# Kernel optimization log

Hardware: AMD Instinct MI355X
Metric: run time of the kernel (lower is better)

## Reference

```python
import jax, jax.numpy as jnp
import numpy as np

G, S, D, H, E = 8, 2048, 1024, 4096, 8  # groups, group_size, d_model, ffn_hidden, experts


def setup_inputs() -> dict:
    key = jax.random.key(0)
    ks = jax.random.split(key, 6)
    s = 0.02
    return {
        "x": jax.random.normal(ks[0], (G, S, D), dtype=jnp.float32),
        "gate_w": jax.random.normal(ks[1], (D, E), dtype=jnp.float32) * s,
        "ew1": jax.random.normal(ks[2], (E, D, H), dtype=jnp.float32) * s,
        "eb1": jnp.zeros((E, H), dtype=jnp.float32),
        "ew2": jax.random.normal(ks[3], (E, H, D), dtype=jnp.float32) * s,
        "eb2": jnp.zeros((E, D), dtype=jnp.float32),
        "sw1": jax.random.normal(ks[4], (D, H), dtype=jnp.float32) * s,
        "sb1": jnp.zeros((H,), dtype=jnp.float32),
        "sw2": jax.random.normal(ks[5], (H, D), dtype=jnp.float32) * s,
        "sb2": jnp.zeros((D,), dtype=jnp.float32),
        "expert_capacity": 2048,
    }


def reference(x, gate_w, ew1, eb1, ew2, eb2, sw1, sb1, sw2, sb2, expert_capacity):
    g, s_, d = x.shape
    e = gate_w.shape[1]
    T = g * s_
    cap = int(expert_capacity)

    # ---- Router (inference path) ----
    router_logits = jnp.einsum('gsd,de->gse', x, gate_w)           # (G,S,E)
    router_probs = jax.nn.softmax(router_logits, axis=-1)
    flat_probs = router_probs.transpose(2, 0, 1).reshape(e, T)      # (E,T)
    pad_w = max(0, cap - T)
    if pad_w > 0:
        flat_probs = jnp.pad(flat_probs, ((0, 0), (0, pad_w)),
                             mode='constant', constant_values=-1e9)
    scores, token_indices = jax.lax.top_k(flat_probs, k=cap)        # (E,C)
    scores = jnp.where(scores > -1e8, scores, 0.0)

    # ---- Routed experts: gather -> grouped FFN -> scale -> scatter-add ----
    x_flat = x.reshape(T, d)                                        # (T,D)
    safe_idx = jnp.clip(token_indices, 0, T - 1)                    # guard padded slots
    toks = x_flat[safe_idx]                                         # (E,C,D)
    h = jax.nn.gelu(jnp.einsum('ecd,edh->ech', toks, ew1) + eb1[:, None, :])
    y = jnp.einsum('ech,ehd->ecd', h, ew2) + eb2[:, None, :]        # (E,C,D)
    y = y * scores[..., None]                                       # zero weight kills padded slots
    routed = jnp.zeros_like(x_flat).at[safe_idx.reshape(-1)].add(y.reshape(-1, d))

    # ---- Shared expert over all tokens ----
    shared = jax.nn.gelu(x_flat @ sw1 + sb1) @ sw2 + sb2            # (T,D)

    return (routed + shared).reshape(g, s_, d)
```

## Files before the change

### kernel.cpp

```cpp
#include <hip/hip_runtime.h>

typedef __bf16 bf16;
typedef __bf16 bf16x8 __attribute__((ext_vector_type(8)));
typedef float f32x4 __attribute__((ext_vector_type(4)));

#define NTOK 16384
#define DMODEL 1024
#define HFFN 4096
#define NEXP 8
#define CAP 2048

#define VMCNT(n) asm volatile("s_waitcnt vmcnt(" #n ")" ::: "memory")
#define LGKM0() do { asm volatile("s_waitcnt lgkmcnt(0)" ::: "memory"); \
                     __builtin_amdgcn_sched_barrier(0); } while (0)
#define BARRIER() __builtin_amdgcn_s_barrier()

__device__ __forceinline__ void gload16(const void* g, void* l) {
  __builtin_amdgcn_global_load_lds((const __attribute__((address_space(1))) void*)g,
                                   (__attribute__((address_space(3))) void*)l, 16, 0, 0);
}

__device__ __forceinline__ float gelu_f(float v) {
  float t = v * v;
  float s2 = v * fmaf(0.10294358f, t, 2.3022084f);
  float e = __builtin_exp2f(-s2);
  return v * __builtin_amdgcn_rcpf(1.0f + e);
}

__device__ __forceinline__ void xcd_remap(int& bx, int& by) {
  const int gx = gridDim.x;
  const int lg = 31 - __clz((unsigned)gx);
  const int w = blockIdx.x + gx * blockIdx.y;
  bx = (w >> 3) & (gx - 1);
  by = (w & 7) | (((w >> 3) >> lg) << 3);
}

__global__ __launch_bounds__(256) void cvt_x_kernel(const float* __restrict__ x,
                                                    bf16* __restrict__ xb) {
  int i = blockIdx.x * blockDim.x + threadIdx.x;
  const float4* a = (const float4*)x + (size_t)i * 2;
  float4 v0 = a[0], v1 = a[1];
  bf16x8 o;
  o[0]=(bf16)v0.x; o[1]=(bf16)v0.y; o[2]=(bf16)v0.z; o[3]=(bf16)v0.w;
  o[4]=(bf16)v1.x; o[5]=(bf16)v1.y; o[6]=(bf16)v1.z; o[7]=(bf16)v1.w;
  *(bf16x8*)(xb + (size_t)i * 8) = o;
}

__global__ __launch_bounds__(64) void router_kernel(const float* __restrict__ x,
                                                    const float* __restrict__ gw,
                                                    float* __restrict__ probs) {
  int t = blockIdx.x;
  int l = threadIdx.x;
  int e = l & 7, chunk = l >> 3;
  const float* xr = x + (size_t)t * DMODEL + chunk * 128;
  const float* gwr = gw + (size_t)(chunk * 128) * NEXP + e;
  float a0 = 0.f, a1 = 0.f;
  #pragma unroll
  for (int d = 0; d < 128; d += 8) {
    float4 xv = *(const float4*)(xr + d);
    float4 xw = *(const float4*)(xr + d + 4);
    a0 += xv.x * gwr[(d+0)*8] + xv.y * gwr[(d+1)*8] + xv.z * gwr[(d+2)*8] + xv.w * gwr[(d+3)*8];
    a1 += xw.x * gwr[(d+4)*8] + xw.y * gwr[(d+5)*8] + xw.z * gwr[(d+6)*8] + xw.w * gwr[(d+7)*8];
  }
  float acc = a0 + a1;
  acc += __shfl_xor(acc, 8);
  acc += __shfl_xor(acc, 16);
  acc += __shfl_xor(acc, 32);
  float m = acc;
  m = fmaxf(m, __shfl_xor(m, 1));
  m = fmaxf(m, __shfl_xor(m, 2));
  m = fmaxf(m, __shfl_xor(m, 4));
  float ex = expf(acc - m);
  float s = ex;
  s += __shfl_xor(s, 1); s += __shfl_xor(s, 2); s += __shfl_xor(s, 4);
  if (l < 8) probs[(size_t)e * NTOK + t] = ex / s;
}

__global__ __launch_bounds__(256) void topk_kernel(const float* __restrict__ probs,
                                                   int* __restrict__ oidx,
                                                   float* __restrict__ oscr) {
  const int e = blockIdx.x;
  const float* p = probs + (size_t)e * NTOK;
  const int t = threadIdx.x;
  __shared__ unsigned hist[256];
  __shared__ unsigned sg[256], sq[256];
  __shared__ unsigned bcast[4];
  unsigned pref = 0, krem = CAP;
  for (int pass = 0; pass < 4; ++pass) {
    const int sh = 24 - pass * 8;
    hist[t] = 0;
    __syncthreads();
    for (int j = 0; j < 64; ++j) {
      unsigned u = __float_as_uint(p[t * 64 + j]);
      bool ok = (pass == 0) || ((u >> (sh + 8)) == pref);
      if (ok) atomicAdd(&hist[(u >> sh) & 255u], 1u);
    }
    __syncthreads();
    if (t == 0) {
      unsigned cum = 0; int b = 255;
      for (; b > 0; --b) {
        unsigned c = hist[b];
        if (cum + c >= krem) break;
        cum += c;
      }
      bcast[0] = (pref << 8) | (unsigned)b;
      bcast[1] = krem - cum;
    }
    __syncthreads();
    pref = bcast[0];
    krem = bcast[1];
  }
  const unsigned thr = pref;
  const unsigned neq_take = krem;
  unsigned cgt = 0, ceq = 0;
  for (int j = 0; j < 64; ++j) {
    unsigned u = __float_as_uint(p[t * 64 + j]);
    cgt += (u > thr);
    ceq += (u == thr);
  }
  sg[t] = cgt; sq[t] = ceq;
  __syncthreads();
  if (t == 0) {
    unsigned ag = 0, aq = 0;
    for (int i = 0; i < 256; ++i) {
      unsigned g = sg[i], q = sq[i];
      sg[i] = ag; sq[i] = aq;
      ag += g; aq += q;
    }
    bcast[2] = ag;
  }
  __syncthreads();
  const unsigned ngt = bcast[2];
  unsigned og = sg[t], oq = sq[t];
  int* oi = oidx + e * CAP;
  float* os = oscr + e * CAP;
  for (int j = 0; j < 64; ++j) {
    int tok = t * 64 + j;
    float pv = p[tok];
    unsigned u = __float_as_uint(pv);
    if (u > thr) {
      oi[og] = tok; os[og] = pv; ++og;
    } else if (u == thr) {
      if (oq < neq_take) { oi[ngt + oq] = tok; os[ngt + oq] = pv; }
      ++oq;
    }
  }
}

__global__ __launch_bounds__(256) void transpose_cvt(const float* __restrict__ in_e,
                                                     const float* __restrict__ in_s,
                                                     bf16* __restrict__ outp,
                                                     int R, int C) {
  int z = blockIdx.z;
  const float* in = (z < 8) ? (in_e + (size_t)z * (size_t)R * C) : in_s;
  bf16* out = outp + (size_t)z * (size_t)R * C;
  __shared__ float tile[64][65];
  int tx = threadIdx.x & 63, ty = threadIdx.x >> 6;
  int c0 = blockIdx.x * 64, r0 = blockIdx.y * 64;
  #pragma unroll
  for (int j = 0; j < 16; ++j) {
    int r = ty + j * 4;
    tile[r][tx] = in[(size_t)(r0 + r) * C + c0 + tx];
  }
  __syncthreads();
  #pragma unroll
  for (int j = 0; j < 16; ++j) {
    int c = ty + j * 4;
    out[(size_t)(c0 + c) * R + r0 + tx] = (bf16)tile[tx][c];
  }
}


#define STAGE_TILE_ALL(tt) do { \
  bf16* D_ = smem + (((tt) & 1) << 15); \
  const int ko_ = (tt) * 64; \
  gload16(srcA0 + ko_, D_ + tid8); \
  gload16(srcA1 + ko_, D_ + 4096 + tid8); \
  gload16(srcA2 + ko_, D_ + 8192 + tid8); \
  gload16(srcA3 + ko_, D_ + 12288 + tid8); \
  gload16(srcB0 + ko_, D_ + 16384 + tid8); \
  gload16(srcB1 + ko_, D_ + 20480 + tid8); \
  gload16(srcB2 + ko_, D_ + 24576 + tid8); \
  gload16(srcB3 + ko_, D_ + 28672 + tid8); \
} while (0)

#define KLOOP8(NT) do { \
  STAGE_TILE_ALL(0); \
  {  \
    bf16* D_ = smem + 32768; \
    gload16(srcA0 + 64, D_ + tid8); \
    gload16(srcA2 + 64, D_ + 8192 + tid8); \
    gload16(srcB0 + 64, D_ + 16384 + tid8); \
    gload16(srcB1 + 64, D_ + 20480 + tid8); \
    gload16(srcB2 + 64, D_ + 24576 + tid8); \
    gload16(srcB3 + 64, D_ + 28672 + tid8); \
  } \
  VMCNT(6); \
  BARRIER(); \
  for (int t = 0; t < (NT); ++t) { \
    const bf16* Ab_ = smem + ((t & 1) << 15); \
    const bf16* Bb_ = Ab_ + 16384; \
    bf16* Scur = smem + ((t & 1) << 15); \
    bf16* Snxt = smem + (((t + 1) & 1) << 15); \
    const int ko1 = (t + 1) * 64, ko2 = (t + 2) * 64; \
    const bool st1 = (t + 1) < (NT), st2 = (t + 2) < (NT); \
    bf16x8 aA[8], aB[8]; \
     \
    _Pragma("unroll") for (int i = 0; i < 4; ++i) { \
      aA[i*2+0] = *(const bf16x8*)(Ab_ + (wr*128 + i*16 + fr)*64 + c0s); \
      aA[i*2+1] = *(const bf16x8*)(Ab_ + (wr*128 + i*16 + fr)*64 + c1s); \
    } \
    _Pragma("unroll") for (int j = 0; j < 2; ++j) { \
      aB[j*2+0] = *(const bf16x8*)(Bb_ + (wc*64 + j*16 + fr)*64 + c0s); \
      aB[j*2+1] = *(const bf16x8*)(Bb_ + (wc*64 + j*16 + fr)*64 + c1s); \
    } \
    if (st1) { \
      gload16(srcA1 + ko1, Snxt + 4096 + tid8); \
      gload16(srcA3 + ko1, Snxt + 12288 + tid8); \
    } \
    BARRIER(); LGKM0(); \
    __builtin_amdgcn_s_setprio(1); \
    _Pragma("unroll") for (int i = 0; i < 4; ++i) \
      _Pragma("unroll") for (int j = 0; j < 2; ++j) { \
        acc[i][j] = __builtin_amdgcn_mfma_f32_16x16x32_bf16(aA[i*2+0], aB[j*2+0], acc[i][j], 0, 0, 0); \
        acc[i][j] = __builtin_amdgcn_mfma_f32_16x16x32_bf16(aA[i*2+1], aB[j*2+1], acc[i][j], 0, 0, 0); \
      } \
    __builtin_amdgcn_s_setprio(0); \
     \
    _Pragma("unroll") for (int j = 0; j < 2; ++j) { \
      aB[4+j*2+0] = *(const bf16x8*)(Bb_ + (wc*64 + 32 + j*16 + fr)*64 + c0s); \
      aB[4+j*2+1] = *(const bf16x8*)(Bb_ + (wc*64 + 32 + j*16 + fr)*64 + c1s); \
    } \
    BARRIER(); LGKM0(); \
    __builtin_amdgcn_s_setprio(1); \
    _Pragma("unroll") for (int i = 0; i < 4; ++i) \
      _Pragma("unroll") for (int j = 0; j < 2; ++j) { \
        acc[i][2+j] = __builtin_amdgcn_mfma_f32_16x16x32_bf16(aA[i*2+0], aB[4+j*2+0], acc[i][2+j], 0, 0, 0); \
        acc[i][2+j] = __builtin_amdgcn_mfma_f32_16x16x32_bf16(aA[i*2+1], aB[4+j*2+1], acc[i][2+j], 0, 0, 0); \
      } \
    __builtin_amdgcn_s_setprio(0); \
     \
    _Pragma("unroll") for (int i = 0; i < 4; ++i) { \
      aA[i*2+0] = *(const bf16x8*)(Ab_ + (wr*128 + 64 + i*16 + fr)*64 + c0s); \
      aA[i*2+1] = *(const bf16x8*)(Ab_ + (wr*128 + 64 + i*16 + fr)*64 + c1s); \
    } \
    if (st2) { \
      gload16(srcA0 + ko2, Scur + tid8); \
      gload16(srcA2 + ko2, Scur + 8192 + tid8); \
    } \
    BARRIER(); LGKM0(); \
    __builtin_amdgcn_s_setprio(1); \
    _Pragma("unroll") for (int i = 0; i < 4; ++i) \
      _Pragma("unroll") for (int j = 0; j < 2; ++j) { \
        acc[4+i][j] = __builtin_amdgcn_mfma_f32_16x16x32_bf16(aA[i*2+0], aB[j*2+0], acc[4+i][j], 0, 0, 0); \
        acc[4+i][j] = __builtin_amdgcn_mfma_f32_16x16x32_bf16(aA[i*2+1], aB[j*2+1], acc[4+i][j], 0, 0, 0); \
      } \
    __builtin_amdgcn_s_setprio(0); \
     \
    if (st2) { \
      gload16(srcB0 + ko2, Scur + 16384 + tid8); \
      gload16(srcB1 + ko2, Scur + 20480 + tid8); \
      gload16(srcB2 + ko2, Scur + 24576 + tid8); \
      gload16(srcB3 + ko2, Scur + 28672 + tid8); \
    } \
    if (st2) { VMCNT(6); } else { VMCNT(0); } \
    BARRIER(); \
    __builtin_amdgcn_s_setprio(1); \
    _Pragma("unroll") for (int i = 0; i < 4; ++i) \
      _Pragma("unroll") for (int j = 0; j < 2; ++j) { \
        acc[4+i][2+j] = __builtin_amdgcn_mfma_f32_16x16x32_bf16(aA[i*2+0], aB[4+j*2+0], acc[4+i][2+j], 0, 0, 0); \
        acc[4+i][2+j] = __builtin_amdgcn_mfma_f32_16x16x32_bf16(aA[i*2+1], aB[4+j*2+1], acc[4+i][2+j], 0, 0, 0); \
      } \
    __builtin_amdgcn_s_setprio(0); \
  } \
} while (0)

__global__ __launch_bounds__(512, 2) void ffn1_gemm(const bf16* __restrict__ xb,
                                                    const bf16* __restrict__ w1t,
                                                    const float* __restrict__ bias1,
                                                    const int* __restrict__ sel,
                                                    bf16* __restrict__ hout,
                                                    int routed) {
  const int e = blockIdx.z;
  const bf16* Bw = w1t + (routed ? (size_t)e * HFFN * DMODEL : 0);
  const float* bias = bias1 + (routed ? (size_t)e * HFFN : 0);
  bf16* hb = hout + (routed ? (size_t)e * CAP * HFFN : 0);
  int bx, by;
  xcd_remap(bx, by);
  const int m0 = by * 256, n0 = bx * 256;
  __shared__ __align__(16) bf16 smem[65536];
  const int tid = threadIdx.x, lane = tid & 63, wave = tid >> 6;
  const int wr = wave >> 2, wc = wave & 3;
  const int tid8 = tid * 8;

  const int srow = tid >> 3, sch = tid & 7;
  const int schs = sch ^ (srow & 7);
  const bf16 *srcA0, *srcA1, *srcA2, *srcA3, *srcB0, *srcB1, *srcB2, *srcB3;
  {
    int ra0 = routed ? sel[e * CAP + m0 + srow]       : (m0 + srow);
    int ra1 = routed ? sel[e * CAP + m0 + 64 + srow]  : (m0 + 64 + srow);
    int ra2 = routed ? sel[e * CAP + m0 + 128 + srow] : (m0 + 128 + srow);
    int ra3 = routed ? sel[e * CAP + m0 + 192 + srow] : (m0 + 192 + srow);
    srcA0 = xb + (size_t)ra0 * DMODEL + schs * 8;
    srcA1 = xb + (size_t)ra1 * DMODEL + schs * 8;
    srcA2 = xb + (size_t)ra2 * DMODEL + schs * 8;
    srcA3 = xb + (size_t)ra3 * DMODEL + schs * 8;
    srcB0 = Bw + (size_t)(n0 + srow) * DMODEL + schs * 8;
    srcB1 = Bw + (size_t)(n0 + 64 + srow) * DMODEL + schs * 8;
    srcB2 = Bw + (size_t)(n0 + 128 + srow) * DMODEL + schs * 8;
    srcB3 = Bw + (size_t)(n0 + 192 + srow) * DMODEL + schs * 8;
  }

  f32x4 acc[8][4];
  #pragma unroll
  for (int i = 0; i < 8; ++i)
    #pragma unroll
    for (int j = 0; j < 4; ++j) acc[i][j] = (f32x4){0.f, 0.f, 0.f, 0.f};

  const int fr = lane & 15;
  const int k8 = lane >> 4;
  const int sw = lane & 7;
  const int c0s = (k8 ^ sw) * 8;
  const int c1s = ((k8 + 4) ^ sw) * 8;

  KLOOP8(DMODEL / 64);

  __syncthreads();
  #pragma unroll
  for (int half = 0; half < 2; ++half) {
    if (wr == half) {
      #pragma unroll
      for (int i = 0; i < 8; ++i) {
        #pragma unroll
        for (int j = 0; j < 4; ++j) {
          const int nl = wc * 64 + j * 16 + fr;
          const float bb = bias[n0 + nl];
          #pragma unroll
          for (int q = 0; q < 4; ++q) {
            const int ml = i * 16 + (lane >> 4) * 4 + q;
            smem[ml * 256 + (nl ^ (((ml >> 2) & 7) << 4))] =
                (bf16)gelu_f(acc[i][j][q] + bb);
          }
        }
      }
    }
    __syncthreads();
    #pragma unroll
    for (int p = 0; p < 8; ++p) {
      const int flat = p * 512 + tid;
      const int row = flat >> 5, nc8 = flat & 31;
      uint4 v = *(const uint4*)(smem + row * 256 + ((nc8 * 8) ^ (((row >> 2) & 7) << 4)));
      *(uint4*)(hb + (size_t)(m0 + half * 128 + row) * HFFN + n0 + nc8 * 8) = v;
    }
    __syncthreads();
  }
}

__global__ __launch_bounds__(512, 2) void ffn2_gemm(const bf16* __restrict__ hbuf,
                                                    const bf16* __restrict__ w2t,
                                                    const float* __restrict__ bias2,
                                                    const int* __restrict__ sel,
                                                    const float* __restrict__ scr,
                                                    float* __restrict__ out,
                                                    int routed) {
  const int e = blockIdx.z;
  const bf16* Ab = hbuf + (routed ? (size_t)e * CAP * HFFN : 0);
  const bf16* Bw = w2t + (routed ? (size_t)e * DMODEL * HFFN : 0);
  const float* bias = bias2 + (routed ? (size_t)e * DMODEL : 0);
  int bx, by;
  xcd_remap(bx, by);
  const int m0 = by * 256, n0 = bx * 256;
  __shared__ __align__(16) bf16 smem[65536];
  __shared__ int s_tok[256];
  __shared__ float s_scl[256];
  const int tid = threadIdx.x, lane = tid & 63, wave = tid >> 6;
  const int wr = wave >> 2, wc = wave & 3;
  const int tid8 = tid * 8;

  const int srow = tid >> 3, sch = tid & 7;
  const int schs = sch ^ (srow & 7);
  const bf16* srcA0 = Ab + (size_t)(m0 + srow) * HFFN + schs * 8;
  const bf16* srcA1 = Ab + (size_t)(m0 + 64 + srow) * HFFN + schs * 8;
  const bf16* srcA2 = Ab + (size_t)(m0 + 128 + srow) * HFFN + schs * 8;
  const bf16* srcA3 = Ab + (size_t)(m0 + 192 + srow) * HFFN + schs * 8;
  const bf16* srcB0 = Bw + (size_t)(n0 + srow) * HFFN + schs * 8;
  const bf16* srcB1 = Bw + (size_t)(n0 + 64 + srow) * HFFN + schs * 8;
  const bf16* srcB2 = Bw + (size_t)(n0 + 128 + srow) * HFFN + schs * 8;
  const bf16* srcB3 = Bw + (size_t)(n0 + 192 + srow) * HFFN + schs * 8;
  if (routed && tid < 256) {
    s_tok[tid] = sel[e * CAP + m0 + tid];
    s_scl[tid] = scr[e * CAP + m0 + tid];
  }

  f32x4 acc[8][4];
  #pragma unroll
  for (int i = 0; i < 8; ++i)
    #pragma unroll
    for (int j = 0; j < 4; ++j) acc[i][j] = (f32x4){0.f, 0.f, 0.f, 0.f};

  const int fr = lane & 15;
  const int k8 = lane >> 4;
  const int sw = lane & 7;
  const int c0s = (k8 ^ sw) * 8;
  const int c1s = ((k8 + 4) ^ sw) * 8;

  KLOOP8(HFFN / 64);

  if (!routed) {
    #pragma unroll
    for (int i = 0; i < 8; ++i) {
      #pragma unroll
      for (int j = 0; j < 4; ++j) {
        const int nl = wc * 64 + j * 16 + fr;
        const float bb = bias[n0 + nl];
        #pragma unroll
        for (int q = 0; q < 4; ++q) {
          const int ml = wr * 128 + i * 16 + (lane >> 4) * 4 + q;
          out[(size_t)(m0 + ml) * DMODEL + n0 + nl] = acc[i][j][q] + bb;
        }
      }
    }
  } else {
    __syncthreads();
    #pragma unroll
    for (int i = 0; i < 8; ++i) {
      #pragma unroll
      for (int j = 0; j < 4; ++j) {
        const int nl = wc * 64 + j * 16 + fr;
        const float bb = bias[n0 + nl];
        #pragma unroll
        for (int q = 0; q < 4; ++q) {
          const int ml = wr * 128 + i * 16 + (lane >> 4) * 4 + q;
          const int tok = s_tok[ml];
          const float sc = s_scl[ml];
          atomicAdd(out + (size_t)tok * DMODEL + n0 + nl, (acc[i][j][q] + bb) * sc);
        }
      }
    }
  }
}

extern "C" void kernel_launch(void* const* d_in, const int* in_sizes, int n_in,
                              void* d_out, int out_size, void* d_ws, size_t ws_size,
                              hipStream_t stream) {
  const float* x   = (const float*)d_in[0];
  const float* gw  = (const float*)d_in[1];
  const float* ew1 = (const float*)d_in[2];
  const float* eb1 = (const float*)d_in[3];
  const float* ew2 = (const float*)d_in[4];
  const float* eb2 = (const float*)d_in[5];
  const float* sw1 = (const float*)d_in[6];
  const float* sb1 = (const float*)d_in[7];
  const float* sw2 = (const float*)d_in[8];
  const float* sb2 = (const float*)d_in[9];
  float* out = (float*)d_out;

  char* ws = (char*)d_ws;
  size_t off = 0;
  bf16* xb      = (bf16*)(ws + off); off += (size_t)NTOK * DMODEL * 2;
  bf16* w1t     = (bf16*)(ws + off); off += (size_t)9 * HFFN * DMODEL * 2;
  bf16* w2t     = (bf16*)(ws + off); off += (size_t)9 * DMODEL * HFFN * 2;
  bf16* hbuf    = (bf16*)(ws + off); off += (size_t)NTOK * HFFN * 2;
  float* probs  = (float*)(ws + off); off += (size_t)NEXP * NTOK * 4;
  int* selidx   = (int*)(ws + off);   off += (size_t)NEXP * CAP * 4;
  float* selscr = (float*)(ws + off); off += (size_t)NEXP * CAP * 4;

  cvt_x_kernel<<<dim3(NTOK * DMODEL / 8 / 256), dim3(256), 0, stream>>>(x, xb);
  router_kernel<<<dim3(NTOK), dim3(64), 0, stream>>>(x, gw, probs);
  topk_kernel<<<dim3(NEXP), dim3(256), 0, stream>>>(probs, selidx, selscr);
  transpose_cvt<<<dim3(HFFN / 64, DMODEL / 64, 9), dim3(256), 0, stream>>>(ew1, sw1, w1t, DMODEL, HFFN);
  transpose_cvt<<<dim3(DMODEL / 64, HFFN / 64, 9), dim3(256), 0, stream>>>(ew2, sw2, w2t, HFFN, DMODEL);

  ffn1_gemm<<<dim3(HFFN / 256, NTOK / 256, 1), dim3(512), 0, stream>>>(
      xb, w1t + (size_t)8 * HFFN * DMODEL, sb1, (const int*)nullptr, hbuf, 0);
  ffn2_gemm<<<dim3(DMODEL / 256, NTOK / 256, 1), dim3(512), 0, stream>>>(
      hbuf, w2t + (size_t)8 * DMODEL * HFFN, sb2, (const int*)nullptr, (const float*)nullptr, out, 0);

  ffn1_gemm<<<dim3(HFFN / 256, CAP / 256, NEXP), dim3(512), 0, stream>>>(
      xb, w1t, eb1, selidx, hbuf, 1);
  ffn2_gemm<<<dim3(DMODEL / 256, CAP / 256, NEXP), dim3(512), 0, stream>>>(
      hbuf, w2t, eb2, selidx, selscr, out, 1);
}
```

Measured before the change: 821.3 us.

## Rework GEMM k-loop into eight-phase quarter-tile double-buffered pipeline

Replaces the KLOOP8 main loop of both FFN GEMMs with a two-iteration unrolled schedule. A and B tiles are staged into LDS in quarters (lo/hi halves of rows), interleaved with eight MFMA sub-blocks per two k-tiles, with vmcnt waits and barriers placed per quarter. Fragment reads for the next sub-block are issued right after each MFMA batch. The row-to-LDS mapping is changed (brow remap, wr*64/wc*32 indexing) so each wave's accumulator blocks still match the unchanged epilogue. The intent is to overlap global-to-LDS loads and LDS reads with MFMA work more finely and hide memory latency. The cost is more barriers and tighter vmcnt accounting, where a wrong count would race.

```diff
diff --git a/kernel.cpp b/kernel.cpp
--- a/kernel.cpp
+++ b/kernel.cpp
@@ -14,6 +14,8 @@
 #define LGKM0() do { asm volatile("s_waitcnt lgkmcnt(0)" ::: "memory"); \
                      __builtin_amdgcn_sched_barrier(0); } while (0)
 #define BARRIER() __builtin_amdgcn_s_barrier()
+#define PRIO1() __builtin_amdgcn_s_setprio(1)
+#define PRIO0() __builtin_amdgcn_s_setprio(0)
 
 __device__ __forceinline__ void gload16(const void* g, void* l) {
   __builtin_amdgcn_global_load_lds((const __attribute__((address_space(1))) void*)g,
@@ -171,107 +173,92 @@
 }
 
 
-#define STAGE_TILE_ALL(tt) do { \
-  bf16* D_ = smem + (((tt) & 1) << 15); \
-  const int ko_ = (tt) * 64; \
-  gload16(srcA0 + ko_, D_ + tid8); \
-  gload16(srcA1 + ko_, D_ + 4096 + tid8); \
-  gload16(srcA2 + ko_, D_ + 8192 + tid8); \
-  gload16(srcA3 + ko_, D_ + 12288 + tid8); \
-  gload16(srcB0 + ko_, D_ + 16384 + tid8); \
-  gload16(srcB1 + ko_, D_ + 20480 + tid8); \
-  gload16(srcB2 + ko_, D_ + 24576 + tid8); \
-  gload16(srcB3 + ko_, D_ + 28672 + tid8); \
-} while (0)
-
-#define KLOOP8(NT) do { \
-  STAGE_TILE_ALL(0); \
-  {  \
-    bf16* D_ = smem + 32768; \
-    gload16(srcA0 + 64, D_ + tid8); \
-    gload16(srcA2 + 64, D_ + 8192 + tid8); \
-    gload16(srcB0 + 64, D_ + 16384 + tid8); \
-    gload16(srcB1 + 64, D_ + 20480 + tid8); \
-    gload16(srcB2 + 64, D_ + 24576 + tid8); \
-    gload16(srcB3 + 64, D_ + 28672 + tid8); \
-  } \
+#define STG_ALO(D, ko) { gload16(srcA0 + (ko), (D) + tid8); gload16(srcA2 + (ko), (D) + 4096 + tid8); }
+#define STG_AHI(D, ko) { gload16(srcA1 + (ko), (D) + 8192 + tid8); gload16(srcA3 + (ko), (D) + 12288 + tid8); }
+#define STG_BLO(D, ko) { gload16(srcBlo0 + (ko), (D) + 16384 + tid8); gload16(srcBlo1 + (ko), (D) + 20480 + tid8); }
+#define STG_BHI(D, ko) { gload16(srcBhi0 + (ko), (D) + 24576 + tid8); gload16(srcBhi1 + (ko), (D) + 28672 + tid8); }
+
+#define RD_A(ARR, D, OFF) \
+  _Pragma("unroll") for (int i = 0; i < 4; ++i) { \
+    ARR[2*i]   = *(const bf16x8*)((D) + (OFF) + (wr*64 + i*16 + fr)*64 + c0s); \
+    ARR[2*i+1] = *(const bf16x8*)((D) + (OFF) + (wr*64 + i*16 + fr)*64 + c1s); \
+  }
+#define RD_B(ARR, D, OFF) \
+  _Pragma("unroll") for (int j = 0; j < 2; ++j) { \
+    ARR[2*j]   = *(const bf16x8*)((D) + (OFF) + (wc*32 + j*16 + fr)*64 + c0s); \
+    ARR[2*j+1] = *(const bf16x8*)((D) + (OFF) + (wc*32 + j*16 + fr)*64 + c1s); \
+  }
+
+#define MFMA_Q(I0, J0, A, B) \
+  _Pragma("unroll") for (int i = 0; i < 4; ++i) \
+    _Pragma("unroll") for (int j = 0; j < 2; ++j) { \
+      acc[(I0)+i][(J0)+j] = __builtin_amdgcn_mfma_f32_16x16x32_bf16((A)[2*i],   (B)[2*j],   acc[(I0)+i][(J0)+j], 0, 0, 0); \
+      acc[(I0)+i][(J0)+j] = __builtin_amdgcn_mfma_f32_16x16x32_bf16((A)[2*i+1], (B)[2*j+1], acc[(I0)+i][(J0)+j], 0, 0, 0); \
+    }
+
+#define KLOOP(NT) do { \
+  bf16* B0_ = smem; \
+  bf16* B1_ = smem + 32768; \
+   \
+  STG_ALO(B0_, 0); STG_BLO(B0_, 0); STG_BHI(B0_, 0); STG_AHI(B0_, 0); \
+  STG_ALO(B1_, 64); STG_BLO(B1_, 64); STG_BHI(B1_, 64); \
   VMCNT(6); \
   BARRIER(); \
-  for (int t = 0; t < (NT); ++t) { \
-    const bf16* Ab_ = smem + ((t & 1) << 15); \
-    const bf16* Bb_ = Ab_ + 16384; \
-    bf16* Scur = smem + ((t & 1) << 15); \
-    bf16* Snxt = smem + (((t + 1) & 1) << 15); \
-    const int ko1 = (t + 1) * 64, ko2 = (t + 2) * 64; \
-    const bool st1 = (t + 1) < (NT), st2 = (t + 2) < (NT); \
-    bf16x8 aA[8], aB[8]; \
-     \
-    _Pragma("unroll") for (int i = 0; i < 4; ++i) { \
-      aA[i*2+0] = *(const bf16x8*)(Ab_ + (wr*128 + i*16 + fr)*64 + c0s); \
-      aA[i*2+1] = *(const bf16x8*)(Ab_ + (wr*128 + i*16 + fr)*64 + c1s); \
-    } \
-    _Pragma("unroll") for (int j = 0; j < 2; ++j) { \
-      aB[j*2+0] = *(const bf16x8*)(Bb_ + (wc*64 + j*16 + fr)*64 + c0s); \
-      aB[j*2+1] = *(const bf16x8*)(Bb_ + (wc*64 + j*16 + fr)*64 + c1s); \
-    } \
-    if (st1) { \
-      gload16(srcA1 + ko1, Snxt + 4096 + tid8); \
-      gload16(srcA3 + ko1, Snxt + 12288 + tid8); \
-    } \
-    BARRIER(); LGKM0(); \
-    __builtin_amdgcn_s_setprio(1); \
-    _Pragma("unroll") for (int i = 0; i < 4; ++i) \
-      _Pragma("unroll") for (int j = 0; j < 2; ++j) { \
-        acc[i][j] = __builtin_amdgcn_mfma_f32_16x16x32_bf16(aA[i*2+0], aB[j*2+0], acc[i][j], 0, 0, 0); \
-        acc[i][j] = __builtin_amdgcn_mfma_f32_16x16x32_bf16(aA[i*2+1], aB[j*2+1], acc[i][j], 0, 0, 0); \
-      } \
-    __builtin_amdgcn_s_setprio(0); \
-     \
-    _Pragma("unroll") for (int j = 0; j < 2; ++j) { \
-      aB[4+j*2+0] = *(const bf16x8*)(Bb_ + (wc*64 + 32 + j*16 + fr)*64 + c0s); \
-      aB[4+j*2+1] = *(const bf16x8*)(Bb_ + (wc*64 + 32 + j*16 + fr)*64 + c1s); \
-    } \
-    BARRIER(); LGKM0(); \
-    __builtin_amdgcn_s_setprio(1); \
-    _Pragma("unroll") for (int i = 0; i < 4; ++i) \
-      _Pragma("unroll") for (int j = 0; j < 2; ++j) { \
-        acc[i][2+j] = __builtin_amdgcn_mfma_f32_16x16x32_bf16(aA[i*2+0], aB[4+j*2+0], acc[i][2+j], 0, 0, 0); \
-        acc[i][2+j] = __builtin_amdgcn_mfma_f32_16x16x32_bf16(aA[i*2+1], aB[4+j*2+1], acc[i][2+j], 0, 0, 0); \
-      } \
-    __builtin_amdgcn_s_setprio(0); \
-     \
-    _Pragma("unroll") for (int i = 0; i < 4; ++i) { \
-      aA[i*2+0] = *(const bf16x8*)(Ab_ + (wr*128 + 64 + i*16 + fr)*64 + c0s); \
-      aA[i*2+1] = *(const bf16x8*)(Ab_ + (wr*128 + 64 + i*16 + fr)*64 + c1s); \
-    } \
-    if (st2) { \
-      gload16(srcA0 + ko2, Scur + tid8); \
-      gload16(srcA2 + ko2, Scur + 8192 + tid8); \
-    } \
-    BARRIER(); LGKM0(); \
-    __builtin_amdgcn_s_setprio(1); \
-    _Pragma("unroll") for (int i = 0; i < 4; ++i) \
-      _Pragma("unroll") for (int j = 0; j < 2; ++j) { \
-        acc[4+i][j] = __builtin_amdgcn_mfma_f32_16x16x32_bf16(aA[i*2+0], aB[j*2+0], acc[4+i][j], 0, 0, 0); \
-        acc[4+i][j] = __builtin_amdgcn_mfma_f32_16x16x32_bf16(aA[i*2+1], aB[j*2+1], acc[4+i][j], 0, 0, 0); \
-      } \
-    __builtin_amdgcn_s_setprio(0); \
-     \
-    if (st2) { \
-      gload16(srcB0 + ko2, Scur + 16384 + tid8); \
-      gload16(srcB1 + ko2, Scur + 20480 + tid8); \
-      gload16(srcB2 + ko2, Scur + 24576 + tid8); \
-      gload16(srcB3 + ko2, Scur + 28672 + tid8); \
-    } \
-    if (st2) { VMCNT(6); } else { VMCNT(0); } \
-    BARRIER(); \
-    __builtin_amdgcn_s_setprio(1); \
-    _Pragma("unroll") for (int i = 0; i < 4; ++i) \
-      _Pragma("unroll") for (int j = 0; j < 2; ++j) { \
-        acc[4+i][2+j] = __builtin_amdgcn_mfma_f32_16x16x32_bf16(aA[i*2+0], aB[4+j*2+0], acc[4+i][2+j], 0, 0, 0); \
-        acc[4+i][2+j] = __builtin_amdgcn_mfma_f32_16x16x32_bf16(aA[i*2+1], aB[4+j*2+1], acc[4+i][2+j], 0, 0, 0); \
-      } \
-    __builtin_amdgcn_s_setprio(0); \
+  RD_A(aA, B0_, 0); RD_B(aB, B0_, 16384); \
+  for (int t = 0; t < (NT); t += 2) { \
+    const bool st = (t + 2) < (NT); \
+    const int ko1 = (t + 1) * 64, ko2 = (t + 2) * 64, ko3 = (t + 3) * 64; \
+     \
+    LGKM0(); \
+    STG_AHI(B1_, ko1); \
+    PRIO1(); MFMA_Q(0, 0, aA, aB); PRIO0(); \
+    if (st) { VMCNT(10); } else { VMCNT(0); } \
+    RD_B(bB, B0_, 24576); \
+    BARRIER(); \
+     \
+    LGKM0(); \
+    if (st) STG_ALO(B0_, ko2); \
+    PRIO1(); MFMA_Q(0, 2, aA, bB); PRIO0(); \
+    if (st) { VMCNT(10); } else { VMCNT(0); } \
+    RD_A(aA, B0_, 8192); \
+    BARRIER(); \
+     \
+    LGKM0(); \
+    if (st) STG_BLO(B0_, ko2); \
+    PRIO1(); MFMA_Q(4, 2, aA, bB); PRIO0(); \
+    BARRIER(); \
+     \
+    LGKM0(); \
+    if (st) STG_BHI(B0_, ko2); \
+    PRIO1(); MFMA_Q(4, 0, aA, aB); PRIO0(); \
+    if (st) { VMCNT(8); } else { VMCNT(0); } \
+    RD_A(aA, B1_, 0); RD_B(aB, B1_, 16384); \
+    BARRIER(); \
+     \
+    LGKM0(); \
+    if (st) STG_AHI(B0_, ko2); \
+    PRIO1(); MFMA_Q(0, 0, aA, aB); PRIO0(); \
+    RD_B(bB, B1_, 24576); \
+    BARRIER(); \
+     \
+    LGKM0(); \
+    if (st) STG_ALO(B1_, ko3); \
+    PRIO1(); MFMA_Q(0, 2, aA, bB); PRIO0(); \
+    if (st) { VMCNT(10); } else { VMCNT(0); } \
+    RD_A(aA, B1_, 8192); \
+    BARRIER(); \
+     \
+    LGKM0(); \
+    if (st) STG_BLO(B1_, ko3); \
+    PRIO1(); MFMA_Q(4, 2, aA, bB); PRIO0(); \
+    BARRIER(); \
+     \
+    LGKM0(); \
+    if (st) STG_BHI(B1_, ko3); \
+    PRIO1(); MFMA_Q(4, 0, aA, aB); PRIO0(); \
+    if (st) { VMCNT(10); } else { VMCNT(0); } \
+    if (st) { RD_A(aA, B0_, 0); RD_B(aB, B0_, 16384); } \
+    BARRIER(); \
   } \
 } while (0)
 
@@ -293,22 +280,23 @@
   const int wr = wave >> 2, wc = wave & 3;
   const int tid8 = tid * 8;
 
-  const int srow = tid >> 3, sch = tid & 7;
-  const int schs = sch ^ (srow & 7);
-  const bf16 *srcA0, *srcA1, *srcA2, *srcA3, *srcB0, *srcB1, *srcB2, *srcB3;
+  const int p = tid >> 3, sch = tid & 7;
+  const int schs = sch ^ (p & 7);
+  const int brow = p + (p & 32);
+  const bf16 *srcA0, *srcA1, *srcA2, *srcA3, *srcBlo0, *srcBlo1, *srcBhi0, *srcBhi1;
   {
-    int ra0 = routed ? sel[e * CAP + m0 + srow]       : (m0 + srow);
-    int ra1 = routed ? sel[e * CAP + m0 + 64 + srow]  : (m0 + 64 + srow);
-    int ra2 = routed ? sel[e * CAP + m0 + 128 + srow] : (m0 + 128 + srow);
-    int ra3 = routed ? sel[e * CAP + m0 + 192 + srow] : (m0 + 192 + srow);
+    int ra0 = routed ? sel[e * CAP + m0 + p]       : (m0 + p);
+    int ra1 = routed ? sel[e * CAP + m0 + 64 + p]  : (m0 + 64 + p);
+    int ra2 = routed ? sel[e * CAP + m0 + 128 + p] : (m0 + 128 + p);
+    int ra3 = routed ? sel[e * CAP + m0 + 192 + p] : (m0 + 192 + p);
     srcA0 = xb + (size_t)ra0 * DMODEL + schs * 8;
     srcA1 = xb + (size_t)ra1 * DMODEL + schs * 8;
     srcA2 = xb + (size_t)ra2 * DMODEL + schs * 8;
     srcA3 = xb + (size_t)ra3 * DMODEL + schs * 8;
-    srcB0 = Bw + (size_t)(n0 + srow) * DMODEL + schs * 8;
-    srcB1 = Bw + (size_t)(n0 + 64 + srow) * DMODEL + schs * 8;
-    srcB2 = Bw + (size_t)(n0 + 128 + srow) * DMODEL + schs * 8;
-    srcB3 = Bw + (size_t)(n0 + 192 + srow) * DMODEL + schs * 8;
+    srcBlo0 = Bw + (size_t)(n0 + brow) * DMODEL + schs * 8;
+    srcBlo1 = srcBlo0 + (size_t)128 * DMODEL;
+    srcBhi0 = srcBlo0 + (size_t)32 * DMODEL;
+    srcBhi1 = srcBlo0 + (size_t)160 * DMODEL;
   }
 
   f32x4 acc[8][4];
@@ -322,8 +310,9 @@
   const int sw = lane & 7;
   const int c0s = (k8 ^ sw) * 8;
   const int c1s = ((k8 + 4) ^ sw) * 8;
-
-  KLOOP8(DMODEL / 64);
+  bf16x8 aA[8], aB[4], bB[4];
+
+  KLOOP(DMODEL / 64);
 
   __syncthreads();
   #pragma unroll
@@ -346,8 +335,8 @@
     }
     __syncthreads();
     #pragma unroll
-    for (int p = 0; p < 8; ++p) {
-      const int flat = p * 512 + tid;
+    for (int pp = 0; pp < 8; ++pp) {
+      const int flat = pp * 512 + tid;
       const int row = flat >> 5, nc8 = flat & 31;
       uint4 v = *(const uint4*)(smem + row * 256 + ((nc8 * 8) ^ (((row >> 2) & 7) << 4)));
       *(uint4*)(hb + (size_t)(m0 + half * 128 + row) * HFFN + n0 + nc8 * 8) = v;
@@ -377,16 +366,17 @@
   const int wr = wave >> 2, wc = wave & 3;
   const int tid8 = tid * 8;
 
-  const int srow = tid >> 3, sch = tid & 7;
-  const int schs = sch ^ (srow & 7);
-  const bf16* srcA0 = Ab + (size_t)(m0 + srow) * HFFN + schs * 8;
-  const bf16* srcA1 = Ab + (size_t)(m0 + 64 + srow) * HFFN + schs * 8;
-  const bf16* srcA2 = Ab + (size_t)(m0 + 128 + srow) * HFFN + schs * 8;
-  const bf16* srcA3 = Ab + (size_t)(m0 + 192 + srow) * HFFN + schs * 8;
-  const bf16* srcB0 = Bw + (size_t)(n0 + srow) * HFFN + schs * 8;
-  const bf16* srcB1 = Bw + (size_t)(n0 + 64 + srow) * HFFN + schs * 8;
-  const bf16* srcB2 = Bw + (size_t)(n0 + 128 + srow) * HFFN + schs * 8;
-  const bf16* srcB3 = Bw + (size_t)(n0 + 192 + srow) * HFFN + schs * 8;
+  const int p = tid >> 3, sch = tid & 7;
+  const int schs = sch ^ (p & 7);
+  const int brow = p + (p & 32);
+  const bf16* srcA0 = Ab + (size_t)(m0 + p) * HFFN + schs * 8;
+  const bf16* srcA1 = Ab + (size_t)(m0 + 64 + p) * HFFN + schs * 8;
+  const bf16* srcA2 = Ab + (size_t)(m0 + 128 + p) * HFFN + schs * 8;
+  const bf16* srcA3 = Ab + (size_t)(m0 + 192 + p) * HFFN + schs * 8;
+  const bf16* srcBlo0 = Bw + (size_t)(n0 + brow) * HFFN + schs * 8;
+  const bf16* srcBlo1 = srcBlo0 + (size_t)128 * HFFN;
+  const bf16* srcBhi0 = srcBlo0 + (size_t)32 * HFFN;
+  const bf16* srcBhi1 = srcBlo0 + (size_t)160 * HFFN;
   if (routed && tid < 256) {
     s_tok[tid] = sel[e * CAP + m0 + tid];
     s_scl[tid] = scr[e * CAP + m0 + tid];
@@ -403,8 +393,9 @@
   const int sw = lane & 7;
   const int c0s = (k8 ^ sw) * 8;
   const int c1s = ((k8 + 4) ^ sw) * 8;
-
-  KLOOP8(HFFN / 64);
+  bf16x8 aA[8], aB[4], bB[4];
+
+  KLOOP(HFFN / 64);
 
   if (!routed) {
     #pragma unroll
```

After: 838.3 us. +2.1%, slower.
